# Kernel tuning notes

Hardware: AMD Instinct MI355X
Metric: run time of the kernel (lower is better)

Reference implementation:

```python
import jax, jax.numpy as jnp
import numpy as np

C = 128
K = 8
B = 2
N = 8192


def setup_inputs() -> dict:
    key = jax.random.key(0)
    ks = jax.random.split(key, 7)
    feats = jax.random.normal(ks[0], (B, N, C), dtype=jnp.float32)
    coords = jax.random.normal(ks[1], (B, N, 3), dtype=jnp.float32)
    scale = 0.02
    Wq = jax.random.normal(ks[2], (C, C), dtype=jnp.float32) * scale
    Wk = jax.random.normal(ks[3], (C, C), dtype=jnp.float32) * scale
    Wv = jax.random.normal(ks[4], (C, C), dtype=jnp.float32) * scale
    Wo = jax.random.normal(ks[5], (C, C), dtype=jnp.float32) * scale
    log_gamma = jnp.log(jnp.float32(0.92))
    return {"feats": feats, "coords": coords, "Wq": Wq, "Wk": Wk,
            "Wv": Wv, "Wo": Wo, "log_gamma": log_gamma}


def _gather_neighbors(points, idx):
    # points: (B,N,C), idx: (B,N,K) -> (B,N,K,C)
    return jax.vmap(lambda p, i: p[i])(points, idx)


def _safe_norm(diff):
    # diff: (...,3) -> (...,) Euclidean norm with zero (not NaN) grad at 0
    d2 = jnp.sum(diff * diff, axis=-1)
    pos = d2 > 0
    return jnp.where(pos, jnp.sqrt(jnp.where(pos, d2, 1.0)), 0.0)


def reference(feats, coords, Wq, Wk, Wv, Wo, log_gamma):
    # nn.Linear(bias=False): y = x @ W.T with W of shape (out, in)
    q = feats @ Wq.T
    k = feats @ Wk.T
    v = feats @ Wv.T

    # KNN via dense pairwise Euclidean distance (mirrors torch.cdist + topk smallest)
    sq = jnp.sum(coords * coords, axis=-1)                      # (B,N)
    d2 = sq[:, :, None] + sq[:, None, :] - 2.0 * jnp.einsum('bnd,bmd->bnm', coords, coords)
    dist_full = jnp.sqrt(jnp.maximum(d2, 0.0))                  # (B,N,N)
    _, idx = jax.lax.top_k(-dist_full, K)                       # (B,N,K) nearest (incl. self)
    idx = jax.lax.stop_gradient(idx)

    k_neigh = _gather_neighbors(k, idx)                         # (B,N,K,C)
    v_neigh = _gather_neighbors(v, idx)                         # (B,N,K,C)
    coord_neigh = _gather_neighbors(coords, idx)                # (B,N,K,3)

    dist = _safe_norm(coords[:, :, None, :] - coord_neigh)      # (B,N,K)
    gamma_w = jnp.exp(log_gamma * dist)                         # (B,N,K)

    scores = jnp.einsum('bnc,bnkc->bnk', q, k_neigh) / (C ** 0.5)
    scores = scores * gamma_w
    weights = jax.nn.softmax(scores, axis=2)                    # (B,N,K)
    agg = jnp.einsum('bnk,bnkc->bnc', weights, v_neigh)         # (B,N,C)
    out = agg @ Wo.T
    return out
```

## Files before the change

### kernel.cpp

```cpp
#include <hip/hip_runtime.h>
#include <math.h>

#define C_DIM 128
#define KNN 8
#define NPTS 8192
#define M_TOTAL 16384
#define CHUNK 1024
#define CAND_CAP 64

typedef unsigned long long u64;

__global__ __launch_bounds__(256) void prep_coords(
    const float* __restrict__ coords, float4* __restrict__ c4) {
  int g = blockIdx.x * 256 + threadIdx.x;
  if (g < M_TOTAL) {
    float x = coords[3 * g + 0];
    float y = coords[3 * g + 1];
    float z = coords[3 * g + 2];
    float s = fmaf(x, x, fmaf(y, y, z * z));
    c4[g] = make_float4(x, y, z, s);
  }
}

__global__ __launch_bounds__(256) void transpose_w(
    const float* __restrict__ Wq, const float* __restrict__ Wk,
    const float* __restrict__ Wv, const float* __restrict__ Wo,
    float* __restrict__ Tq, float* __restrict__ Tk,
    float* __restrict__ Tv, float* __restrict__ To) {
  int g = blockIdx.x * 256 + threadIdx.x;
  int mat = g >> 14;
  int j = g & 16383;
  int c = j >> 7, o = j & 127;
  const float* src = (mat == 0) ? Wq : (mat == 1) ? Wk : (mat == 2) ? Wv : Wo;
  float* dst = (mat == 0) ? Tq : (mat == 1) ? Tk : (mat == 2) ? Tv : To;
  dst[j] = src[o * C_DIM + c];
}

__device__ __forceinline__ void stage_x64(
    float (*Xs)[132], const float* __restrict__ X, int row0, int t) {
  const float4* X4 = (const float4*)(X + (size_t)row0 * C_DIM);
  for (int i = t; i < 64 * 32; i += 256) {
    int r = i >> 5, c4i = i & 31;
    *(float4*)&Xs[r][c4i * 4] = X4[i];
  }
}

__global__ __launch_bounds__(256) void gemm_qkv(
    const float* __restrict__ X,
    const float* __restrict__ WTq, const float* __restrict__ WTk,
    const float* __restrict__ WTv,
    float* __restrict__ Yq, float* __restrict__ Yk, float* __restrict__ Yv) {
  __shared__ float Xs[64][132];
  const int t = threadIdx.x;
  const int row0 = (blockIdx.x >> 1) * 64;
  const int ob = (blockIdx.x & 1) * 64;
  stage_x64(Xs, X, row0, t);
  __syncthreads();

  const int r0 = (t >> 4) * 4;
  const int o0 = ob + (t & 15) * 4;

  float aq[4][4], ak[4][4], av[4][4];
#pragma unroll
  for (int i = 0; i < 4; ++i)
#pragma unroll
    for (int j = 0; j < 4; ++j) { aq[i][j] = 0.f; ak[i][j] = 0.f; av[i][j] = 0.f; }

  for (int c = 0; c < C_DIM; c += 4) {
    float xs[4][4];
#pragma unroll
    for (int i = 0; i < 4; ++i) {
      float4 xv = *(const float4*)&Xs[r0 + i][c];
      xs[i][0] = xv.x; xs[i][1] = xv.y; xs[i][2] = xv.z; xs[i][3] = xv.w;
    }
#pragma unroll
    for (int cc = 0; cc < 4; ++cc) {
      const size_t wrow = (size_t)(c + cc) * C_DIM + o0;
      float4 qa = *(const float4*)&WTq[wrow];
      float4 ka = *(const float4*)&WTk[wrow];
      float4 va = *(const float4*)&WTv[wrow];
#pragma unroll
      for (int i = 0; i < 4; ++i) {
        float x = xs[i][cc];
        aq[i][0] = fmaf(x, qa.x, aq[i][0]); aq[i][1] = fmaf(x, qa.y, aq[i][1]);
        aq[i][2] = fmaf(x, qa.z, aq[i][2]); aq[i][3] = fmaf(x, qa.w, aq[i][3]);
        ak[i][0] = fmaf(x, ka.x, ak[i][0]); ak[i][1] = fmaf(x, ka.y, ak[i][1]);
        ak[i][2] = fmaf(x, ka.z, ak[i][2]); ak[i][3] = fmaf(x, ka.w, ak[i][3]);
        av[i][0] = fmaf(x, va.x, av[i][0]); av[i][1] = fmaf(x, va.y, av[i][1]);
        av[i][2] = fmaf(x, va.z, av[i][2]); av[i][3] = fmaf(x, va.w, av[i][3]);
      }
    }
  }

#pragma unroll
  for (int i = 0; i < 4; ++i) {
    const size_t yoff = (size_t)(row0 + r0 + i) * C_DIM + o0;
    *(float4*)&Yq[yoff] = make_float4(aq[i][0], aq[i][1], aq[i][2], aq[i][3]);
    *(float4*)&Yk[yoff] = make_float4(ak[i][0], ak[i][1], ak[i][2], ak[i][3]);
    *(float4*)&Yv[yoff] = make_float4(av[i][0], av[i][1], av[i][2], av[i][3]);
  }
}

__global__ __launch_bounds__(256) void gemm_xwt(
    const float* __restrict__ X, const float* __restrict__ WT,
    float* __restrict__ Y) {
  __shared__ float Xs[64][132];
  const int t = threadIdx.x;
  const int row0 = (blockIdx.x >> 1) * 64;
  const int ob = (blockIdx.x & 1) * 64;
  stage_x64(Xs, X, row0, t);
  __syncthreads();

  const int r0 = (t >> 4) * 4;
  const int o0 = ob + (t & 15) * 4;

  float acc[4][4];
#pragma unroll
  for (int i = 0; i < 4; ++i)
#pragma unroll
    for (int j = 0; j < 4; ++j) acc[i][j] = 0.0f;

  for (int c = 0; c < C_DIM; c += 4) {
    float xs[4][4];
#pragma unroll
    for (int i = 0; i < 4; ++i) {
      float4 xv = *(const float4*)&Xs[r0 + i][c];
      xs[i][0] = xv.x; xs[i][1] = xv.y; xs[i][2] = xv.z; xs[i][3] = xv.w;
    }
#pragma unroll
    for (int cc = 0; cc < 4; ++cc) {
      const size_t wrow = (size_t)(c + cc) * C_DIM + o0;
      float4 wa = *(const float4*)&WT[wrow];
#pragma unroll
      for (int i = 0; i < 4; ++i) {
        float x = xs[i][cc];
        acc[i][0] = fmaf(x, wa.x, acc[i][0]); acc[i][1] = fmaf(x, wa.y, acc[i][1]);
        acc[i][2] = fmaf(x, wa.z, acc[i][2]); acc[i][3] = fmaf(x, wa.w, acc[i][3]);
      }
    }
  }

#pragma unroll
  for (int i = 0; i < 4; ++i) {
    float* yrow = Y + (size_t)(row0 + r0 + i) * C_DIM + o0;
    *(float4*)yrow = make_float4(acc[i][0], acc[i][1], acc[i][2], acc[i][3]);
  }
}

__device__ __forceinline__ u64 wave_min_u64(u64 x) {
#pragma unroll
  for (int off = 32; off > 0; off >>= 1) {
    u64 o = __shfl_xor(x, off, 64);
    x = (o < x) ? o : x;
  }
  return x;
}

__device__ __forceinline__ float wave_8th_of_top2(float u0, float u1) {
  float m = 0.0f;
#pragma unroll
  for (int r = 0; r < KNN; ++r) {
    m = u0;
#pragma unroll
    for (int off = 32; off > 0; off >>= 1) {
      float o = __shfl_xor(m, off, 64);
      m = fminf(m, o);
    }
    bool mine = (u0 == m);
    u0 = mine ? u1 : u0;
    u1 = mine ? INFINITY : u1;
  }
  return m;
}

__global__ __launch_bounds__(256) void knn_attn(
    const float4* __restrict__ c4,
    const float* __restrict__ q, const float* __restrict__ k,
    const float* __restrict__ v, const float* __restrict__ log_gamma_p,
    float* __restrict__ agg) {
  __shared__ float4 pts[CHUNK];
  __shared__ u64 cand[4][CAND_CAP];

  const int t = threadIdx.x;
  const int wave = t >> 6;
  const int lane = t & 63;
  const int qi = blockIdx.x * 4 + wave;
  const int b = qi >> 13;
  const int n = qi & (NPTS - 1);
  const int base = b * NPTS;

  const float4 qp = c4[base + n];
  const u64 lmask = (1ull << lane) - 1ull;

  float m1 = INFINITY, m2 = INFINITY;

  for (int ch = 0; ch < NPTS / CHUNK; ++ch) {
    __syncthreads();
    for (int i = t; i < CHUNK; i += 256) pts[i] = c4[base + ch * CHUNK + i];
    __syncthreads();

#pragma unroll
    for (int it = 0; it < CHUNK / 128; ++it) {
      const int ml = it * 128 + lane;
      const float4 pa = pts[ml];
      const float4 pb = pts[ml + 64];
      float dota = fmaf(qp.x, pa.x, fmaf(qp.y, pa.y, qp.z * pa.z));
      float dotb = fmaf(qp.x, pb.x, fmaf(qp.y, pb.y, qp.z * pb.z));
      float d2a = fmaxf(qp.w + pa.w - 2.0f * dota, 0.0f);
      float d2b = fmaxf(qp.w + pb.w - 2.0f * dotb, 0.0f);
      float h;
      h = fmaxf(m1, d2a); m1 = fminf(m1, d2a); m2 = fminf(m2, h);
      h = fmaxf(m1, d2b); m1 = fminf(m1, d2b); m2 = fminf(m2, h);
    }
  }

  const float tau = wave_8th_of_top2(m1, m2);

  int cnt = 0;
  for (int ch = 0; ch < NPTS / CHUNK; ++ch) {
    __syncthreads();
    for (int i = t; i < CHUNK; i += 256) pts[i] = c4[base + ch * CHUNK + i];
    __syncthreads();

#pragma unroll
    for (int it = 0; it < CHUNK / 128; ++it) {
      const int ml = it * 128 + lane;
      const float4 pa = pts[ml];
      const float4 pb = pts[ml + 64];
      float dota = fmaf(qp.x, pa.x, fmaf(qp.y, pa.y, qp.z * pa.z));
      float dotb = fmaf(qp.x, pb.x, fmaf(qp.y, pb.y, qp.z * pb.z));
      float d2a = fmaxf(qp.w + pa.w - 2.0f * dota, 0.0f);
      float d2b = fmaxf(qp.w + pb.w - 2.0f * dotb, 0.0f);
      bool ga = d2a <= tau;
      bool gb = d2b <= tau;
      u64 mska = __ballot(ga);
      u64 mskb = __ballot(gb);
      if (mska | mskb) {
        const unsigned ia = (unsigned)(ch * CHUNK + ml);
        if (ga) {
          int pos = cnt + (int)__popcll(mska & lmask);
          if (pos < CAND_CAP)
            cand[wave][pos] = ((u64)__float_as_uint(d2a) << 32) | ia;
        }
        cnt += (int)__popcll(mska);
        if (gb) {
          int pos = cnt + (int)__popcll(mskb & lmask);
          if (pos < CAND_CAP)
            cand[wave][pos] = ((u64)__float_as_uint(d2b) << 32) | (ia + 64);
        }
        cnt += (int)__popcll(mskb);
      }
    }
  }

  const int m_ = (cnt < CAND_CAP) ? cnt : CAND_CAP;
  u64 mykey = (lane < m_) ? cand[wave][lane] : ~0ull;
  int ni_[KNN];
#pragma unroll
  for (int r = 0; r < KNN; ++r) {
    u64 mm = wave_min_u64(mykey);
    ni_[r] = (int)(unsigned)(mm & 0xFFFFFFFFu);
    if (mykey == mm) mykey = ~0ull;
  }

  const float lg = *log_gamma_p;
  const size_t qrow = (size_t)(base + n) * C_DIM;
  const float qv0 = q[qrow + lane];
  const float qv1 = q[qrow + lane + 64];

  float score[KNN];
#pragma unroll
  for (int j = 0; j < KNN; ++j) {
    const int mj = ni_[j];
    const size_t krow = (size_t)(base + mj) * C_DIM;
    float p = fmaf(qv1, k[krow + lane + 64], qv0 * k[krow + lane]);
#pragma unroll
    for (int off = 32; off > 0; off >>= 1) p += __shfl_xor(p, off, 64);
    const float4 pm = c4[base + mj];
    float dx = qp.x - pm.x, dy = qp.y - pm.y, dz = qp.z - pm.z;
    float d2p = fmaf(dx, dx, fmaf(dy, dy, dz * dz));
    float dist = d2p > 0.0f ? sqrtf(d2p) : 0.0f;
    float gw = expf(lg * dist);
    score[j] = (p / 11.313708498984761f) * gw;
  }

  float mx = score[0];
#pragma unroll
  for (int j = 1; j < KNN; ++j) mx = fmaxf(mx, score[j]);
  float w[KNN]; float sum = 0.0f;
#pragma unroll
  for (int j = 0; j < KNN; ++j) { w[j] = expf(score[j] - mx); sum += w[j]; }
#pragma unroll
  for (int j = 0; j < KNN; ++j) w[j] = w[j] / sum;

  float a0 = 0.0f, a1 = 0.0f;
#pragma unroll
  for (int j = 0; j < KNN; ++j) {
    const size_t vrow = (size_t)(base + ni_[j]) * C_DIM;
    a0 = fmaf(w[j], v[vrow + lane], a0);
    a1 = fmaf(w[j], v[vrow + lane + 64], a1);
  }
  agg[qrow + lane] = a0;
  agg[qrow + lane + 64] = a1;
}

extern "C" void kernel_launch(void* const* d_in, const int* in_sizes, int n_in,
                              void* d_out, int out_size, void* d_ws, size_t ws_size,
                              hipStream_t stream) {
  const float* feats  = (const float*)d_in[0];
  const float* coords = (const float*)d_in[1];
  const float* Wq     = (const float*)d_in[2];
  const float* Wk     = (const float*)d_in[3];
  const float* Wv     = (const float*)d_in[4];
  const float* Wo     = (const float*)d_in[5];
  const float* lg     = (const float*)d_in[6];
  float* out = (float*)d_out;

  float* ws = (float*)d_ws;
  const size_t ROWS = (size_t)M_TOTAL * C_DIM;
  float*  q   = ws;
  float*  k   = ws + ROWS;
  float*  v   = ws + 2 * ROWS;
  float4* c4  = (float4*)(ws + 3 * ROWS);
  float*  WTq = ws + 3 * ROWS + 4 * (size_t)M_TOTAL;
  float*  WTk = WTq + C_DIM * C_DIM;
  float*  WTv = WTk + C_DIM * C_DIM;
  float*  WTo = WTv + C_DIM * C_DIM;
  float*  agg = q;

  prep_coords<<<M_TOTAL / 256, 256, 0, stream>>>(coords, c4);
  transpose_w<<<256, 256, 0, stream>>>(Wq, Wk, Wv, Wo, WTq, WTk, WTv, WTo);
  gemm_qkv<<<M_TOTAL / 32, 256, 0, stream>>>(feats, WTq, WTk, WTv, q, k, v);
  knn_attn<<<M_TOTAL / 4, 256, 0, stream>>>(c4, q, k, v, lg, agg);
  gemm_xwt<<<M_TOTAL / 32, 256, 0, stream>>>(agg, WTo, out);
}
```

Baseline: 218.7 us.

## Estimate KNN threshold from a point sample and widen candidate buffer

The first full pass over all points, which computed a distance threshold, is replaced by a scan of only the first 2048 points read straight from global memory. The resulting threshold is looser, so the candidate buffer grows to 96 entries. Each lane now holds two sorted keys for the wave-level top-8 selection. This removes most of the threshold pass. The risk is candidate overflow, and therefore wrong neighbors, when many points fall under the loose threshold.

```diff
diff --git a/kernel.cpp b/kernel.cpp
--- a/kernel.cpp
+++ b/kernel.cpp
@@ -6,7 +6,8 @@
 #define NPTS 8192
 #define M_TOTAL 16384
 #define CHUNK 1024
-#define CAND_CAP 64
+#define SAMPLE 2048
+#define CAND_CAP 96
 
 typedef unsigned long long u64;
 
@@ -193,27 +194,14 @@
   const u64 lmask = (1ull << lane) - 1ull;
 
   float m1 = INFINITY, m2 = INFINITY;
-
-  for (int ch = 0; ch < NPTS / CHUNK; ++ch) {
-    __syncthreads();
-    for (int i = t; i < CHUNK; i += 256) pts[i] = c4[base + ch * CHUNK + i];
-    __syncthreads();
-
-#pragma unroll
-    for (int it = 0; it < CHUNK / 128; ++it) {
-      const int ml = it * 128 + lane;
-      const float4 pa = pts[ml];
-      const float4 pb = pts[ml + 64];
-      float dota = fmaf(qp.x, pa.x, fmaf(qp.y, pa.y, qp.z * pa.z));
-      float dotb = fmaf(qp.x, pb.x, fmaf(qp.y, pb.y, qp.z * pb.z));
-      float d2a = fmaxf(qp.w + pa.w - 2.0f * dota, 0.0f);
-      float d2b = fmaxf(qp.w + pb.w - 2.0f * dotb, 0.0f);
-      float h;
-      h = fmaxf(m1, d2a); m1 = fminf(m1, d2a); m2 = fminf(m2, h);
-      h = fmaxf(m1, d2b); m1 = fminf(m1, d2b); m2 = fminf(m2, h);
-    }
-  }
-
+  const float4* cb = c4 + base;
+#pragma unroll 4
+  for (int it = 0; it < SAMPLE / 64; ++it) {
+    const float4 p = cb[it * 64 + lane];
+    float dot = fmaf(qp.x, p.x, fmaf(qp.y, p.y, qp.z * p.z));
+    float d2 = fmaxf(qp.w + p.w - 2.0f * dot, 0.0f);
+    float h = fmaxf(m1, d2); m1 = fminf(m1, d2); m2 = fminf(m2, h);
+  }
   const float tau = wave_8th_of_top2(m1, m2);
 
   int cnt = 0;
@@ -254,13 +242,15 @@
   }
 
   const int m_ = (cnt < CAND_CAP) ? cnt : CAND_CAP;
-  u64 mykey = (lane < m_) ? cand[wave][lane] : ~0ull;
+  u64 a = (lane < m_) ? cand[wave][lane] : ~0ull;
+  u64 bb = (lane + 64 < m_) ? cand[wave][lane + 64] : ~0ull;
+  u64 k0 = (a < bb) ? a : bb, k1 = (a < bb) ? bb : a;
   int ni_[KNN];
 #pragma unroll
   for (int r = 0; r < KNN; ++r) {
-    u64 mm = wave_min_u64(mykey);
+    u64 mm = wave_min_u64(k0);
     ni_[r] = (int)(unsigned)(mm & 0xFFFFFFFFu);
-    if (mykey == mm) mykey = ~0ull;
+    if (k0 == mm) { k0 = k1; k1 = ~0ull; }
   }
 
   const float lg = *log_gamma_p;
```

Result: faster. 196.4 us (-10.2%).
